# Kernel tuning notes

Hardware: AMD Instinct MI355X
Metric: run time of the kernel (lower is better)

## Reference

```python
import jax, jax.numpy as jnp
import numpy as np
from jax import lax

B_, C_IN, IMG, P = 32, 3, 224, 16
D, DEPTH, NCLS = 384, 24, 1000
DI, DS, DCONV, DTR = 2 * D, 16, 4, 24  # d_inner, d_state, d_conv, dt_rank
L = (IMG // P) ** 2 + 1  # 197 tokens incl. cls


def setup_inputs() -> dict:
    key = jax.random.key(0)
    ks = jax.random.split(key, 20)
    s = 0.02
    inp = {
        "x": jax.random.normal(ks[0], (B_, C_IN, IMG, IMG), jnp.float32),
        "patch_w": jax.random.normal(ks[1], (D, C_IN, P, P), jnp.float32) * s,
        "patch_b": jnp.zeros((D,), jnp.float32),
        "cls_token": jax.random.normal(ks[2], (1, 1, D), jnp.float32) * s,
        "pos_embed": jax.random.normal(ks[3], (1, L, D), jnp.float32) * s,
        "ln_w": jnp.ones((DEPTH, D), jnp.float32),
        "ln_b": jnp.zeros((DEPTH, D), jnp.float32),
        "in_proj_w": jax.random.normal(ks[4], (DEPTH, 2 * DI, D), jnp.float32) * s,
        "conv1d_w": jax.random.normal(ks[5], (DEPTH, DI, DCONV), jnp.float32) * s,
        "conv1d_b": jnp.zeros((DEPTH, DI), jnp.float32),
        "x_proj_w": jax.random.normal(ks[6], (DEPTH, DTR + 2 * DS, DI), jnp.float32) * s,
        "dt_proj_w": jax.random.normal(ks[7], (DEPTH, DI, DTR), jnp.float32) * 0.1,
        "dt_proj_b": jax.random.uniform(ks[8], (DEPTH, DI), jnp.float32, -4.0, -2.0),
        "A_log": jnp.tile(jnp.log(jnp.arange(1, DS + 1, dtype=jnp.float32))[None, None, :], (DEPTH, DI, 1)),
        "D_param": jnp.ones((DEPTH, DI), jnp.float32),
        "out_proj_w": jax.random.normal(ks[9], (DEPTH, D, DI), jnp.float32) * s,
        "normf_w": jnp.ones((D,), jnp.float32),
        "normf_b": jnp.zeros((D,), jnp.float32),
        "head_w": jax.random.normal(ks[10], (NCLS, D), jnp.float32) * s,
        "head_b": jnp.zeros((NCLS,), jnp.float32),
    }
    return inp


def _layernorm(x, w, b, eps=1e-5):
    mu = jnp.mean(x, -1, keepdims=True)
    var = jnp.mean(jnp.square(x - mu), -1, keepdims=True)
    return (x - mu) * lax.rsqrt(var + eps) * w + b


def _silu(x):
    return x * jax.nn.sigmoid(x)


def _selective_scan(dA, dBx, Cm):
    # dA, dBx: [B, L, DI, DS]; Cm: [B, L, DS] -> y: [B, L, DI]
    def step(h, inp):
        a, bx, c = inp
        h = a * h + bx
        return h, jnp.einsum("bds,bs->bd", h, c)

    h0 = jnp.zeros((dA.shape[0], DI, DS), dA.dtype)
    _, ys = lax.scan(step, h0, (dA.swapaxes(0, 1), dBx.swapaxes(0, 1), Cm.swapaxes(0, 1)))
    return ys.swapaxes(0, 1)


def _mamba_block(h, p):
    (ln_w, ln_b, in_w, cw, cb, xp_w, dtw, dtb, A_log, Dp, ow) = p
    x = _layernorm(h, ln_w, ln_b)               # [B,L,D]
    xz = jnp.einsum("bld,ed->ble", x, in_w)      # [B,L,2*DI]
    xb, z = jnp.split(xz, 2, axis=-1)
    # causal depthwise conv1d, kernel DCONV
    xc = xb.swapaxes(1, 2)                       # [B,DI,L]
    xc = lax.conv_general_dilated(xc, cw[:, None, :], (1,), [(DCONV - 1, 0)],
                                  feature_group_count=DI,
                                  dimension_numbers=("NCH", "OIH", "NCH"))
    xb = _silu(xc.swapaxes(1, 2) + cb)           # [B,L,DI]
    xdbl = jnp.einsum("bld,ed->ble", xb, xp_w)   # [B,L,DTR+2*DS]
    dt, Bm, Cm = jnp.split(xdbl, [DTR, DTR + DS], axis=-1)
    dt = jax.nn.softplus(jnp.einsum("blr,dr->bld", dt, dtw) + dtb)  # [B,L,DI]
    A = -jnp.exp(A_log)                          # [DI,DS]
    dA = jnp.exp(dt[..., None] * A)              # [B,L,DI,DS]
    dBx = dt[..., None] * Bm[:, :, None, :] * xb[..., None]
    y = _selective_scan(dA, dBx, Cm) + Dp * xb
    y = y * _silu(z)
    out = jnp.einsum("ble,de->bld", y, ow)       # [B,L,D]
    return h + out, None


def reference(x, patch_w, patch_b, cls_token, pos_embed, ln_w, ln_b, in_proj_w,
              conv1d_w, conv1d_b, x_proj_w, dt_proj_w, dt_proj_b, A_log, D_param,
              out_proj_w, normf_w, normf_b, head_w, head_b):
    B = x.shape[0]
    feat = lax.conv_general_dilated(x, patch_w, (P, P), "VALID",
                                    dimension_numbers=("NCHW", "OIHW", "NCHW"))
    feat = feat.reshape(B, D, -1).swapaxes(1, 2) + patch_b  # [B,196,D]
    tok = jnp.concatenate([jnp.broadcast_to(cls_token, (B, 1, D)), feat], axis=1)
    tok = tok + pos_embed
    layer_params = (ln_w, ln_b, in_proj_w, conv1d_w, conv1d_b, x_proj_w,
                    dt_proj_w, dt_proj_b, A_log, D_param, out_proj_w)
    tok, _ = lax.scan(_mamba_block, tok, layer_params)
    tok = _layernorm(tok, normf_w, normf_b)
    return tok[:, 0] @ head_w.T + head_b  # [B, NCLS]
```

## Files before the change

### kernel.cpp

```cpp
#include <hip/hip_runtime.h>
#include <math.h>

#define B_    32
#define D_    384
#define DEPTH 24
#define DI    768
#define DS    16
#define DCONV 4
#define DTR   24
#define L_    197
#define LPAD  208
#define NCLS  1000
#define NTOK  (B_*L_)
#define MPAD  6400
#define NCOMB 896

typedef __bf16 bf16;
typedef __bf16 bf16x2 __attribute__((ext_vector_type(2)));
typedef __bf16 bf16x4 __attribute__((ext_vector_type(4)));
typedef __bf16 bf16x8 __attribute__((ext_vector_type(8)));
typedef float  floatx4 __attribute__((ext_vector_type(4)));

#define INW_E  (1536*384)
#define OUTW_E (384*768)
#define PW_E   (384*768)
#define HW_E   (1024*384)

__device__ __forceinline__ float sigmoidf_(float x){ return 1.f/(1.f+__expf(-x)); }

template<int CTRL>
__device__ __forceinline__ float dppf_(float x){
    return __int_as_float(__builtin_amdgcn_update_dpp(0, __float_as_int(x), CTRL, 0xF, 0xF, true));
}
template<int M>
__device__ __forceinline__ float sxor_(float x){
    if constexpr (M==1)      return dppf_<0xB1>(x);
    else if constexpr (M==2) return dppf_<0x4E>(x);
    else if constexpr (M==4) return dppf_<0x1B>(dppf_<0x141>(x));
    else                     return dppf_<0x128>(x);
}
template<int M>
__device__ __forceinline__ void rlevel_(float* v, const int s){
    const bool hi = (s & M) != 0;
    #pragma unroll
    for (int i = 0; i < M; ++i) {
        const float keep = hi ? v[i+M] : v[i];
        const float send = hi ? v[i] : v[i+M];
        v[i] = keep + sxor_<M>(send);
    }
}

__global__ void wconv_all_kernel(const float* __restrict__ in_w, const float* __restrict__ out_w,
                                 const float* __restrict__ patch_w, const float* __restrict__ head_w,
                                 bf16* __restrict__ w_in_b, bf16* __restrict__ w_out_b,
                                 bf16* __restrict__ pw_b, bf16* __restrict__ hw_b)
{
    long idx = (long)blockIdx.x*256 + threadIdx.x;
    if (idx < (long)DEPTH*INW_E) { w_in_b[idx] = (bf16)in_w[idx]; return; }
    idx -= (long)DEPTH*INW_E;
    if (idx < (long)DEPTH*OUTW_E) { w_out_b[idx] = (bf16)out_w[idx]; return; }
    idx -= (long)DEPTH*OUTW_E;
    if (idx < PW_E) { pw_b[idx] = (bf16)patch_w[idx]; return; }
    idx -= PW_E;
    if (idx < HW_E) hw_b[idx] = (idx < (long)NCLS*384) ? (bf16)head_w[idx] : (bf16)0.f;
}

__global__ void wcomb_kernel(const float* __restrict__ dtw, const float* __restrict__ xpw,
                             bf16* __restrict__ wc)
{
    __shared__ float sw[24];
    const int o = blockIdx.x;
    if (o < 768) {
        if (threadIdx.x < 24) sw[threadIdx.x] = dtw[(long)o*DTR + threadIdx.x];
        __syncthreads();
        for (int i = threadIdx.x; i < DI; i += 256) {
            float acc = 0.f;
            #pragma unroll
            for (int r = 0; r < 24; ++r) acc += sw[r]*xpw[r*DI + i];
            wc[(long)o*DI + i] = (bf16)acc;
        }
    } else if (o < 800) {
        const float* src = xpw + (long)(o - 768 + 24)*DI;
        for (int i = threadIdx.x; i < DI; i += 256) wc[(long)o*DI + i] = (bf16)src[i];
    } else {
        for (int i = threadIdx.x; i < DI; i += 256) wc[(long)o*DI + i] = (bf16)0.f;
    }
}

__global__ void im2col_kernel(const float* __restrict__ x, bf16* __restrict__ patches)
{
    const long idx = (long)blockIdx.x*256 + threadIdx.x;
    if (idx >= (long)B_*196*768) return;
    const int k = idx % 768;
    const int prow = idx / 768;
    const int b = prow / 196, pi = prow % 196;
    const int ph = pi / 14, pw = pi % 14;
    const int c = k >> 8, rem = k & 255, ii = rem >> 4, jj = rem & 15;
    patches[((long)(b*L_ + 1 + pi))*768 + k] =
        (bf16)x[(((long)b*3 + c)*224 + ph*16 + ii)*224 + pw*16 + jj];
}

__global__ void add_pos_kernel(float* __restrict__ tok, const float* __restrict__ pb,
                               const float* __restrict__ pos, const float* __restrict__ cls)
{
    const int idx = blockIdx.x*256 + threadIdx.x;
    if (idx >= NTOK*D_) return;
    const int dd = idx % D_;
    const int row = idx / D_;
    const int p = row % L_;
    if (p == 0) tok[idx] = cls[dd] + pos[dd];
    else        tok[idx] += pb[dd] + pos[p*D_ + dd];
}

template<typename OUT_T>
__global__ void ln_kernel(const float* __restrict__ x, const float* __restrict__ w,
                          const float* __restrict__ b, OUT_T* __restrict__ out,
                          int rows, int xstride, int ostride)
{
    const int row = blockIdx.x*blockDim.y + threadIdx.y;
    if (row >= rows) return;
    const int lane = threadIdx.x;
    const float* xr = x + (long)row*xstride;
    float v[6]; float s = 0.f;
    #pragma unroll
    for (int i = 0; i < 6; ++i) { v[i] = xr[lane + 64*i]; s += v[i]; }
    #pragma unroll
    for (int o = 32; o; o >>= 1) s += __shfl_xor(s, o, 64);
    const float mu = s * (1.f/384.f);
    float var = 0.f;
    #pragma unroll
    for (int i = 0; i < 6; ++i) { float d = v[i]-mu; var += d*d; }
    #pragma unroll
    for (int o = 32; o; o >>= 1) var += __shfl_xor(var, o, 64);
    const float rstd = rsqrtf(var*(1.f/384.f) + 1e-5f);
    OUT_T* orow = out + (long)row*ostride;
    #pragma unroll
    for (int i = 0; i < 6; ++i) { int c = lane + 64*i; orow[c] = (OUT_T)((v[i]-mu)*rstd*w[c] + b[c]); }
}

template<int BM, int ACC, typename CT>
__global__ __launch_bounds__(256)
void gemm_bf16_kernel(const bf16* __restrict__ A, const bf16* __restrict__ B,
                      CT* __restrict__ C, int M, int N, int K)
{
    constexpr int ASLABS = BM/16;
    constexpr int NJ = (BM == 128) ? 4 : 2;
    __shared__ bf16 As[BM*32];
    __shared__ bf16 Bs[128*32];
    const int tid  = threadIdx.x;
    const int wave = tid >> 6, lane = tid & 63;
    const int bm = blockIdx.x*BM, bn = blockIdx.y*128;
    const int wm = (BM == 128) ? (wave>>1)*64 : 0;
    const int wn = (BM == 128) ? (wave&1)*64 : wave*32;
    floatx4 acc[4][NJ];
    #pragma unroll
    for (int i=0;i<4;++i)
        #pragma unroll
        for (int j=0;j<NJ;++j) acc[i][j] = (floatx4){0.f,0.f,0.f,0.f};

    const int lrow = lane >> 2;
    const int lcol = (lane & 3) * 8;
    const int am = lane & 15, ak = (lane>>4)*8;

    for (int k0 = 0; k0 < K; k0 += 32) {
        #pragma unroll
        for (int s = wave; s < ASLABS + 8; s += 4) {
            if (s < ASLABS) {
                const bf16* ga = A + (long)(bm + s*16 + lrow)*K + k0 + lcol;
                __builtin_amdgcn_global_load_lds(
                    (const __attribute__((address_space(1))) void*)ga,
                    (__attribute__((address_space(3))) void*)(As + s*512), 16, 0, 0);
            } else {
                const int s2 = s - ASLABS;
                const bf16* gb = B + (long)(bn + s2*16 + lrow)*K + k0 + lcol;
                __builtin_amdgcn_global_load_lds(
                    (const __attribute__((address_space(1))) void*)gb,
                    (__attribute__((address_space(3))) void*)(Bs + s2*512), 16, 0, 0);
            }
        }
        __syncthreads();
        bf16x8 af[4], bff[NJ];
        #pragma unroll
        for (int i=0;i<4;++i) af[i]  = *(const bf16x8*)(As + (wm + i*16 + am)*32 + ak);
        #pragma unroll
        for (int j=0;j<NJ;++j) bff[j] = *(const bf16x8*)(Bs + (wn + j*16 + am)*32 + ak);
        #pragma unroll
        for (int i=0;i<4;++i)
            #pragma unroll
            for (int j=0;j<NJ;++j)
                acc[i][j] = __builtin_amdgcn_mfma_f32_16x16x32_bf16(af[i], bff[j], acc[i][j], 0, 0, 0);
        __syncthreads();
    }
    const int rbase = bm + wm + (lane>>4)*4;
    const int cbase = bn + wn + (lane & 15);
    #pragma unroll
    for (int i = 0; i < 4; ++i) {
        #pragma unroll
        for (int r = 0; r < 4; ++r) {
            const int row = rbase + i*16 + r;
            if (row >= M) continue;
            #pragma unroll
            for (int j = 0; j < NJ; ++j) {
                const long idx = (long)row*N + cbase + j*16;
                if (ACC) C[idx] += acc[i][j][r];
                else     C[idx]  = (CT)acc[i][j][r];
            }
        }
    }
}

__global__ void conv_silu_kernel(const bf16* __restrict__ xz, const float* __restrict__ cw,
                                 const float* __restrict__ cb, bf16* __restrict__ out)
{
    const int idx = blockIdx.x*256 + threadIdx.x;
    if (idx >= NTOK*(DI/2)) return;
    const int dp = idx % (DI/2);
    const int bl = idx / (DI/2);
    const int l  = bl % L_;
    const int di = dp*2;
    const long rowbase = (long)(bl - l)*(2*DI) + di;
    const float4 wa = *(const float4*)(cw + di*4);
    const float4 wb = *(const float4*)(cw + di*4 + 4);
    float a0 = cb[di], a1 = cb[di+1];
    #pragma unroll
    for (int k = 0; k < 4; ++k) {
        const int lt = l - 3 + k;
        if (lt >= 0) {
            const bf16x2 xv = *(const bf16x2*)(xz + rowbase + (long)lt*(2*DI));
            const float w0 = (k==0)?wa.x:(k==1)?wa.y:(k==2)?wa.z:wa.w;
            const float w1 = (k==0)?wb.x:(k==1)?wb.y:(k==2)?wb.z:wb.w;
            a0 += w0 * (float)xv[0];
            a1 += w1 * (float)xv[1];
        }
    }
    bf16x2 r;
    r[0] = (bf16)(a0 * sigmoidf_(a0));
    r[1] = (bf16)(a1 * sigmoidf_(a1));
    *(bf16x2*)(out + (long)bl*DI + di) = r;
}

__global__ __launch_bounds__(256)
void scan_kernel(const bf16* __restrict__ xbc, const bf16* __restrict__ comb,
                 const bf16* __restrict__ xz, const float* __restrict__ A_log,
                 const float* __restrict__ Dp, const float* __restrict__ dtb,
                 bf16* __restrict__ y)
{
    const int tid  = threadIdx.x;
    const int w    = tid >> 6, lane = tid & 63;
    const int s    = lane & 15;
    const int dlq  = lane >> 4;
    const int dl   = w*4 + dlq;
    const int bx   = blockIdx.x;
    const int cblk = (bx & 7)*6 + (bx >> 3);
    const int di0  = cblk*16;
    const int di   = di0 + dl;
    const int b    = blockIdx.y;

    const float A_s = -__expf(A_log[di*DS + s]);
    const float Dv  = Dp[di];

    __shared__ __align__(16) float2 sh_dt2[(LPAD/2)*32];
    __shared__ __align__(16) bf16x2 sh_bc2[(LPAD/2)*32];
    __shared__ bf16x2 sh_xz[LPAD*16];

    const long base = (long)b*L_;
    const int e = tid & 15;
    const float bias = dtb[di0 + e];
    for (int idx = tid; idx < LPAD*16; idx += 256) {
        const int t = idx >> 4;
        const int idx2 = (t >> 1)*32 + 2*e + (t & 1);
        float2 dtdx = {0.f, 0.f};
        bf16x2 bc;  bc[0] = (bf16)0.f; bc[1] = (bf16)0.f;
        bf16x2 xzv; xzv[0] = (bf16)0.f; xzv[1] = (bf16)0.f;
        if (t < L_) {
            const long row = base + t;
            const float xv = (float)xbc[row*DI + di0 + e];
            const float zv = (float)xz[row*(2*DI) + DI + di0 + e];
            const float dr = (float)comb[row*NCOMB + di0 + e] + bias;
            const float dtv = (dr > 20.f) ? dr : __logf(1.f + __expf(dr));
            dtdx.x = dtv; dtdx.y = dtv*xv;
            bc[0] = comb[row*NCOMB + 768 + e];
            bc[1] = comb[row*NCOMB + 784 + e];
            xzv[0] = (bf16)xv; xzv[1] = (bf16)zv;
        }
        sh_dt2[idx2] = dtdx;
        sh_bc2[idx2] = bc;
        sh_xz[idx]   = xzv;
    }
    __syncthreads();

    const float4* dt4 = (const float4*)sh_dt2;
    const bf16x4* bc4 = (const bf16x4*)sh_bc2;

    float h = 0.f;
    for (int c = 0; c < LPAD/16; ++c) {
        float v[16];
        #pragma unroll
        for (int t2 = 0; t2 < 8; ++t2) {
            const int g2 = c*8 + t2;
            const float4 q  = dt4[g2*16 + dl];
            const bf16x4 bc = bc4[g2*16 + s];
            const float a0 = __expf(q.x * A_s);
            h = fmaf(a0, h, q.y * (float)bc[0]);
            v[2*t2]   = h * (float)bc[1];
            const float a1 = __expf(q.z * A_s);
            h = fmaf(a1, h, q.w * (float)bc[2]);
            v[2*t2+1] = h * (float)bc[3];
        }
        rlevel_<8>(v, s); rlevel_<4>(v, s); rlevel_<2>(v, s); rlevel_<1>(v, s);
        const int gt = c*16 + s;
        if (gt < L_) {
            const bf16x2 xzv = sh_xz[gt*16 + dl];
            const float xv = (float)xzv[0], z = (float)xzv[1];
            y[(base + gt)*DI + di] = (bf16)((v[0] + Dv*xv) * z * sigmoidf_(z));
        }
    }
}

__global__ void head_bias_kernel(const float* __restrict__ chead, const float* __restrict__ hb,
                                 float* __restrict__ out)
{
    const int idx = blockIdx.x*256 + threadIdx.x;
    if (idx >= B_*NCLS) return;
    const int n = idx % NCLS, b = idx / NCLS;
    out[idx] = chead[(long)b*1024 + n] + hb[n];
}

extern "C" void kernel_launch(void* const* d_in, const int* in_sizes, int n_in,
                              void* d_out, int out_size, void* d_ws, size_t ws_size,
                              hipStream_t stream)
{
    const float* x       = (const float*)d_in[0];
    const float* patch_w = (const float*)d_in[1];
    const float* patch_b = (const float*)d_in[2];
    const float* cls_tok = (const float*)d_in[3];
    const float* pos_emb = (const float*)d_in[4];
    const float* ln_w    = (const float*)d_in[5];
    const float* ln_b    = (const float*)d_in[6];
    const float* in_w    = (const float*)d_in[7];
    const float* conv_w  = (const float*)d_in[8];
    const float* conv_b  = (const float*)d_in[9];
    const float* xp_w    = (const float*)d_in[10];
    const float* dt_w    = (const float*)d_in[11];
    const float* dt_b    = (const float*)d_in[12];
    const float* A_log   = (const float*)d_in[13];
    const float* D_par   = (const float*)d_in[14];
    const float* out_w   = (const float*)d_in[15];
    const float* normf_w = (const float*)d_in[16];
    const float* normf_b = (const float*)d_in[17];
    const float* head_w  = (const float*)d_in[18];
    const float* head_b  = (const float*)d_in[19];
    float* out = (float*)d_out;

    char* p = (char*)d_ws;
    float* tok    = (float*)p;  p += (long)NTOK*D_*4;
    bf16*  xz_b   = (bf16*)p;   p += (long)MPAD*2*DI*2;
    bf16*  xbc_b  = (bf16*)p;   p += (long)MPAD*DI*2;
    bf16*  y_b    = (bf16*)p;   p += (long)MPAD*DI*2;
    bf16*  comb_b = (bf16*)p;   p += (long)MPAD*NCOMB*2;
    bf16*  xnorm_b= (bf16*)p;   p += (long)MPAD*D_*2;
    bf16*  ln0_b  = (bf16*)p;   p += (long)64*D_*2;
    float* chead  = (float*)p;  p += (long)64*1024*4;
    bf16*  wcomb_b= (bf16*)p;   p += (long)NCOMB*DI*2;
    bf16*  w_in_b = (bf16*)p;   p += (long)DEPTH*INW_E*2;
    bf16*  w_out_b= (bf16*)p;   p += (long)DEPTH*OUTW_E*2;
    bf16*  pw_b   = (bf16*)p;   p += (long)PW_E*2;
    bf16*  hw_b   = (bf16*)p;   p += (long)HW_E*2;
    bf16*  patches = comb_b;

    const long WCONV_E = (long)DEPTH*(INW_E + OUTW_E) + PW_E + HW_E;
    wconv_all_kernel<<<dim3((WCONV_E + 255)/256), 256, 0, stream>>>(
        in_w, out_w, patch_w, head_w, w_in_b, w_out_b, pw_b, hw_b);

    im2col_kernel<<<dim3(((long)B_*196*768 + 255)/256), 256, 0, stream>>>(x, patches);
    gemm_bf16_kernel<64,0,float><<<dim3(100, 3), 256, 0, stream>>>(
        patches, pw_b, tok, NTOK, D_, 768);
    add_pos_kernel<<<dim3((NTOK*D_ + 255)/256), 256, 0, stream>>>(tok, patch_b, pos_emb, cls_tok);

    for (int layer = 0; layer < DEPTH; ++layer) {
        ln_kernel<bf16><<<dim3(NTOK/4), dim3(64,4), 0, stream>>>(
            tok, ln_w + layer*D_, ln_b + layer*D_, xnorm_b, NTOK, D_, D_);
        gemm_bf16_kernel<128,0,bf16><<<dim3(50, 12), 256, 0, stream>>>(
            xnorm_b, w_in_b + (long)layer*INW_E, xz_b, NTOK, 2*DI, D_);
        conv_silu_kernel<<<dim3((NTOK*(DI/2) + 255)/256), 256, 0, stream>>>(
            xz_b, conv_w + layer*DI*DCONV, conv_b + layer*DI, xbc_b);
        wcomb_kernel<<<dim3(NCOMB), 256, 0, stream>>>(
            dt_w + (long)layer*DI*DTR, xp_w + (long)layer*56*768, wcomb_b);
        gemm_bf16_kernel<128,0,bf16><<<dim3(50, 7), 256, 0, stream>>>(
            xbc_b, wcomb_b, comb_b, NTOK, NCOMB, DI);
        scan_kernel<<<dim3(48, B_), 256, 0, stream>>>(
            xbc_b, comb_b, xz_b, A_log + layer*DI*DS, D_par + layer*DI,
            dt_b + layer*DI, y_b);
        gemm_bf16_kernel<64,1,float><<<dim3(100, 3), 256, 0, stream>>>(
            y_b, w_out_b + (long)layer*OUTW_E, tok, NTOK, D_, DI);
    }

    ln_kernel<bf16><<<dim3(8), dim3(64,4), 0, stream>>>(tok, normf_w, normf_b, ln0_b, B_, L_*D_, D_);
    gemm_bf16_kernel<64,0,float><<<dim3(1, 8), 256, 0, stream>>>(
        ln0_b, hw_b, chead, 64, 1024, D_);
    head_bias_kernel<<<dim3((B_*NCLS + 255)/256), 256, 0, stream>>>(chead, head_b, out);
}
```

Measured before the change: 3.352 ms.

## Vectorize weight conversion and conv, fuse LN with wcomb, bf16 scan staging

Several unrelated changes land together. The weight-conversion kernel and the depthwise conv+SiLU kernel now process 8 elements per thread with vector loads and stores. The per-layer layernorm and the dt/x_proj weight-combination kernel are merged into one launch, saving one launch per layer. The scan kernel stores dt and dt*x in shared memory as bf16 instead of fp32 and uses exp2 with a prescaled A. The bf16 staging lowers shared-memory traffic but costs precision in the recurrence.

```diff
diff --git a/kernel.cpp b/kernel.cpp
--- a/kernel.cpp
+++ b/kernel.cpp
@@ -50,40 +50,78 @@
     }
 }
 
+#define INW_ALL  ((long)DEPTH*INW_E)
+#define OUTW_ALL ((long)DEPTH*OUTW_E)
+#define WCONV_TOT (INW_ALL + OUTW_ALL + PW_E + HW_E)
 __global__ void wconv_all_kernel(const float* __restrict__ in_w, const float* __restrict__ out_w,
                                  const float* __restrict__ patch_w, const float* __restrict__ head_w,
                                  bf16* __restrict__ w_in_b, bf16* __restrict__ w_out_b,
                                  bf16* __restrict__ pw_b, bf16* __restrict__ hw_b)
 {
-    long idx = (long)blockIdx.x*256 + threadIdx.x;
-    if (idx < (long)DEPTH*INW_E) { w_in_b[idx] = (bf16)in_w[idx]; return; }
-    idx -= (long)DEPTH*INW_E;
-    if (idx < (long)DEPTH*OUTW_E) { w_out_b[idx] = (bf16)out_w[idx]; return; }
-    idx -= (long)DEPTH*OUTW_E;
-    if (idx < PW_E) { pw_b[idx] = (bf16)patch_w[idx]; return; }
-    idx -= PW_E;
-    if (idx < HW_E) hw_b[idx] = (idx < (long)NCLS*384) ? (bf16)head_w[idx] : (bf16)0.f;
-}
-
-__global__ void wcomb_kernel(const float* __restrict__ dtw, const float* __restrict__ xpw,
-                             bf16* __restrict__ wc)
-{
-    __shared__ float sw[24];
-    const int o = blockIdx.x;
-    if (o < 768) {
-        if (threadIdx.x < 24) sw[threadIdx.x] = dtw[(long)o*DTR + threadIdx.x];
-        __syncthreads();
-        for (int i = threadIdx.x; i < DI; i += 256) {
-            float acc = 0.f;
-            #pragma unroll
-            for (int r = 0; r < 24; ++r) acc += sw[r]*xpw[r*DI + i];
-            wc[(long)o*DI + i] = (bf16)acc;
-        }
-    } else if (o < 800) {
-        const float* src = xpw + (long)(o - 768 + 24)*DI;
-        for (int i = threadIdx.x; i < DI; i += 256) wc[(long)o*DI + i] = (bf16)src[i];
+    long idx = ((long)blockIdx.x*256 + threadIdx.x)*8;
+    if (idx >= WCONV_TOT) return;
+    const float* src; bf16* dst; long off;
+    bool pad = false;
+    if (idx < INW_ALL)                { src = in_w;  dst = w_in_b;  off = idx; }
+    else if (idx < INW_ALL+OUTW_ALL)  { src = out_w; dst = w_out_b; off = idx - INW_ALL; }
+    else if (idx < INW_ALL+OUTW_ALL+PW_E) { src = patch_w; dst = pw_b; off = idx - INW_ALL - OUTW_ALL; }
+    else { off = idx - INW_ALL - OUTW_ALL - PW_E; src = head_w; dst = hw_b; pad = (off >= (long)NCLS*384); }
+    bf16x8 r;
+    if (pad) {
+        #pragma unroll
+        for (int j = 0; j < 8; ++j) r[j] = (bf16)0.f;
     } else {
-        for (int i = threadIdx.x; i < DI; i += 256) wc[(long)o*DI + i] = (bf16)0.f;
+        const float4 a = *(const float4*)(src + off);
+        const float4 c = *(const float4*)(src + off + 4);
+        r[0]=(bf16)a.x; r[1]=(bf16)a.y; r[2]=(bf16)a.z; r[3]=(bf16)a.w;
+        r[4]=(bf16)c.x; r[5]=(bf16)c.y; r[6]=(bf16)c.z; r[7]=(bf16)c.w;
+    }
+    *(bf16x8*)(dst + off) = r;
+}
+
+__global__ void ln_wcomb_kernel(const float* __restrict__ x, const float* __restrict__ w,
+                                const float* __restrict__ b, bf16* __restrict__ out,
+                                const float* __restrict__ dtw, const float* __restrict__ xpw,
+                                bf16* __restrict__ wc)
+{
+    if (blockIdx.x < NTOK/4) {
+        const int row = blockIdx.x*4 + threadIdx.y;
+        const int lane = threadIdx.x;
+        const float* xr = x + (long)row*D_;
+        float v[6]; float s = 0.f;
+        #pragma unroll
+        for (int i = 0; i < 6; ++i) { v[i] = xr[lane + 64*i]; s += v[i]; }
+        #pragma unroll
+        for (int o = 32; o; o >>= 1) s += __shfl_xor(s, o, 64);
+        const float mu = s * (1.f/384.f);
+        float var = 0.f;
+        #pragma unroll
+        for (int i = 0; i < 6; ++i) { float d = v[i]-mu; var += d*d; }
+        #pragma unroll
+        for (int o = 32; o; o >>= 1) var += __shfl_xor(var, o, 64);
+        const float rstd = rsqrtf(var*(1.f/384.f) + 1e-5f);
+        bf16* orow = out + (long)row*D_;
+        #pragma unroll
+        for (int i = 0; i < 6; ++i) { int c = lane + 64*i; orow[c] = (bf16)((v[i]-mu)*rstd*w[c] + b[c]); }
+    } else {
+        const int o = blockIdx.x - NTOK/4;
+        const int tid = threadIdx.y*64 + threadIdx.x;
+        if (o < 768) {
+            __shared__ float sw[24];
+            if (tid < 24) sw[tid] = dtw[(long)o*DTR + tid];
+            __syncthreads();
+            for (int i = tid; i < DI; i += 256) {
+                float acc = 0.f;
+                #pragma unroll
+                for (int r = 0; r < 24; ++r) acc += sw[r]*xpw[r*DI + i];
+                wc[(long)o*DI + i] = (bf16)acc;
+            }
+        } else if (o < 800) {
+            const float* src = xpw + (long)(o - 768 + 24)*DI;
+            for (int i = tid; i < DI; i += 256) wc[(long)o*DI + i] = (bf16)src[i];
+        } else {
+            for (int i = tid; i < DI; i += 256) wc[(long)o*DI + i] = (bf16)0.f;
+        }
     }
 }
 
@@ -213,30 +251,32 @@
                                  const float* __restrict__ cb, bf16* __restrict__ out)
 {
     const int idx = blockIdx.x*256 + threadIdx.x;
-    if (idx >= NTOK*(DI/2)) return;
-    const int dp = idx % (DI/2);
-    const int bl = idx / (DI/2);
+    if (idx >= NTOK*96) return;
+    const int g  = idx % 96;
+    const int bl = idx / 96;
     const int l  = bl % L_;
-    const int di = dp*2;
+    const int di = g*8;
     const long rowbase = (long)(bl - l)*(2*DI) + di;
-    const float4 wa = *(const float4*)(cw + di*4);
-    const float4 wb = *(const float4*)(cw + di*4 + 4);
-    float a0 = cb[di], a1 = cb[di+1];
+    bf16x8 xv[4];
     #pragma unroll
     for (int k = 0; k < 4; ++k) {
         const int lt = l - 3 + k;
         if (lt >= 0) {
-            const bf16x2 xv = *(const bf16x2*)(xz + rowbase + (long)lt*(2*DI));
-            const float w0 = (k==0)?wa.x:(k==1)?wa.y:(k==2)?wa.z:wa.w;
-            const float w1 = (k==0)?wb.x:(k==1)?wb.y:(k==2)?wb.z:wb.w;
-            a0 += w0 * (float)xv[0];
-            a1 += w1 * (float)xv[1];
-        }
-    }
-    bf16x2 r;
-    r[0] = (bf16)(a0 * sigmoidf_(a0));
-    r[1] = (bf16)(a1 * sigmoidf_(a1));
-    *(bf16x2*)(out + (long)bl*DI + di) = r;
+            xv[k] = *(const bf16x8*)(xz + rowbase + (long)lt*(2*DI));
+        } else {
+            #pragma unroll
+            for (int j = 0; j < 8; ++j) xv[k][j] = (bf16)0.f;
+        }
+    }
+    bf16x8 r;
+    #pragma unroll
+    for (int j = 0; j < 8; ++j) {
+        const float4 wj = ((const float4*)cw)[di + j];
+        float a = cb[di + j];
+        a += wj.x*(float)xv[0][j] + wj.y*(float)xv[1][j] + wj.z*(float)xv[2][j] + wj.w*(float)xv[3][j];
+        r[j] = (bf16)(a * sigmoidf_(a));
+    }
+    *(bf16x8*)(out + (long)bl*DI + di) = r;
 }
 
 __global__ __launch_bounds__(256)
@@ -256,10 +296,10 @@
     const int di   = di0 + dl;
     const int b    = blockIdx.y;
 
-    const float A_s = -__expf(A_log[di*DS + s]);
-    const float Dv  = Dp[di];
-
-    __shared__ __align__(16) float2 sh_dt2[(LPAD/2)*32];
+    const float A2_s = -__expf(A_log[di*DS + s]) * 1.44269504f;
+    const float Dv   = Dp[di];
+
+    __shared__ __align__(16) bf16x2 sh_dt2[(LPAD/2)*32];
     __shared__ __align__(16) bf16x2 sh_bc2[(LPAD/2)*32];
     __shared__ bf16x2 sh_xz[LPAD*16];
 
@@ -269,16 +309,16 @@
     for (int idx = tid; idx < LPAD*16; idx += 256) {
         const int t = idx >> 4;
         const int idx2 = (t >> 1)*32 + 2*e + (t & 1);
-        float2 dtdx = {0.f, 0.f};
-        bf16x2 bc;  bc[0] = (bf16)0.f; bc[1] = (bf16)0.f;
-        bf16x2 xzv; xzv[0] = (bf16)0.f; xzv[1] = (bf16)0.f;
+        bf16x2 dtdx; dtdx[0] = (bf16)0.f; dtdx[1] = (bf16)0.f;
+        bf16x2 bc;   bc[0] = (bf16)0.f;   bc[1] = (bf16)0.f;
+        bf16x2 xzv;  xzv[0] = (bf16)0.f;  xzv[1] = (bf16)0.f;
         if (t < L_) {
             const long row = base + t;
             const float xv = (float)xbc[row*DI + di0 + e];
             const float zv = (float)xz[row*(2*DI) + DI + di0 + e];
             const float dr = (float)comb[row*NCOMB + di0 + e] + bias;
             const float dtv = (dr > 20.f) ? dr : __logf(1.f + __expf(dr));
-            dtdx.x = dtv; dtdx.y = dtv*xv;
+            dtdx[0] = (bf16)dtv; dtdx[1] = (bf16)(dtv*xv);
             bc[0] = comb[row*NCOMB + 768 + e];
             bc[1] = comb[row*NCOMB + 784 + e];
             xzv[0] = (bf16)xv; xzv[1] = (bf16)zv;
@@ -289,7 +329,7 @@
     }
     __syncthreads();
 
-    const float4* dt4 = (const float4*)sh_dt2;
+    const bf16x4* dt4 = (const bf16x4*)sh_dt2;
     const bf16x4* bc4 = (const bf16x4*)sh_bc2;
 
     float h = 0.f;
@@ -298,13 +338,13 @@
         #pragma unroll
         for (int t2 = 0; t2 < 8; ++t2) {
             const int g2 = c*8 + t2;
-            const float4 q  = dt4[g2*16 + dl];
+            const bf16x4 q  = dt4[g2*16 + dl];
             const bf16x4 bc = bc4[g2*16 + s];
-            const float a0 = __expf(q.x * A_s);
-            h = fmaf(a0, h, q.y * (float)bc[0]);
+            const float a0 = __builtin_amdgcn_exp2f((float)q[0] * A2_s);
+            h = fmaf(a0, h, (float)q[1] * (float)bc[0]);
             v[2*t2]   = h * (float)bc[1];
-            const float a1 = __expf(q.z * A_s);
-            h = fmaf(a1, h, q.w * (float)bc[2]);
+            const float a1 = __builtin_amdgcn_exp2f((float)q[2] * A2_s);
+            h = fmaf(a1, h, (float)q[3] * (float)bc[2]);
             v[2*t2+1] = h * (float)bc[3];
         }
         rlevel_<8>(v, s); rlevel_<4>(v, s); rlevel_<2>(v, s); rlevel_<1>(v, s);
@@ -368,8 +408,7 @@
     bf16*  hw_b   = (bf16*)p;   p += (long)HW_E*2;
     bf16*  patches = comb_b;
 
-    const long WCONV_E = (long)DEPTH*(INW_E + OUTW_E) + PW_E + HW_E;
-    wconv_all_kernel<<<dim3((WCONV_E + 255)/256), 256, 0, stream>>>(
+    wconv_all_kernel<<<dim3((WCONV_TOT/8 + 255)/256), 256, 0, stream>>>(
         in_w, out_w, patch_w, head_w, w_in_b, w_out_b, pw_b, hw_b);
 
     im2col_kernel<<<dim3(((long)B_*196*768 + 255)/256), 256, 0, stream>>>(x, patches);
@@ -378,14 +417,13 @@
     add_pos_kernel<<<dim3((NTOK*D_ + 255)/256), 256, 0, stream>>>(tok, patch_b, pos_emb, cls_tok);
 
     for (int layer = 0; layer < DEPTH; ++layer) {
-        ln_kernel<bf16><<<dim3(NTOK/4), dim3(64,4), 0, stream>>>(
-            tok, ln_w + layer*D_, ln_b + layer*D_, xnorm_b, NTOK, D_, D_);
+        ln_wcomb_kernel<<<dim3(NTOK/4 + NCOMB), dim3(64,4), 0, stream>>>(
+            tok, ln_w + layer*D_, ln_b + layer*D_, xnorm_b,
+            dt_w + (long)layer*DI*DTR, xp_w + (long)layer*56*768, wcomb_b);
         gemm_bf16_kernel<128,0,bf16><<<dim3(50, 12), 256, 0, stream>>>(
             xnorm_b, w_in_b + (long)layer*INW_E, xz_b, NTOK, 2*DI, D_);
-        conv_silu_kernel<<<dim3((NTOK*(DI/2) + 255)/256), 256, 0, stream>>>(
+        conv_silu_kernel<<<dim3((NTOK*96 + 255)/256), 256, 0, stream>>>(
             xz_b, conv_w + layer*DI*DCONV, conv_b + layer*DI, xbc_b);
-        wcomb_kernel<<<dim3(NCOMB), 256, 0, stream>>>(
-            dt_w + (long)layer*DI*DTR, xp_w + (long)layer*56*768, wcomb_b);
         gemm_bf16_kernel<128,0,bf16><<<dim3(50, 7), 256, 0, stream>>>(
             xbc_b, wcomb_b, comb_b, NTOK, NCOMB, DI);
         scan_kernel<<<dim3(48, B_), 256, 0, stream>>>(
```

After: 3.142 ms. 1.07x faster.
